# Optimization experiments

Measured on AMD Instinct MI355X. Metric: run time of the kernel, lower is better.

The kernel has to match this reference:

```python
import jax, jax.numpy as jnp
import numpy as np

FEAT_STRIDE = 16
SCALES = np.array([2.0, 4.0, 8.0, 16.0])
RATIOS = np.array([0.5, 1.0, 2.0])
TIME_DIM = (16, 12, 8, 4)
S = 16            # sample_duration
A = 12            # anchors per location = len(scales)*len(ratios)
PRE = 2000        # RPN_PRE_NMS_TOP_N (TEST)
POST = 300        # RPN_POST_NMS_TOP_N (TEST)
THRESH = 0.7      # RPN_NMS_THRESH


def _whctrs(a):
    w = a[2] - a[0] + 1.0
    h = a[3] - a[1] + 1.0
    return w, h, a[0] + 0.5 * (w - 1), a[1] + 0.5 * (h - 1)


def _mkanchors(ws, hs, xc, yc):
    ws = ws[:, None]; hs = hs[:, None]
    return np.hstack((xc - 0.5 * (ws - 1), yc - 0.5 * (hs - 1),
                      xc + 0.5 * (ws - 1), yc + 0.5 * (hs - 1)))


def generate_anchors(base_size=16):
    base = np.array([1.0, 1.0, base_size, base_size]) - 1
    w, h, xc, yc = _whctrs(base)
    ws = np.round(np.sqrt(w * h / RATIOS)); hs = np.round(ws * RATIOS)
    ratio_anchors = _mkanchors(ws, hs, xc, yc)
    rows = []
    for i in range(ratio_anchors.shape[0]):
        wi, hi, xi, yi = _whctrs(ratio_anchors[i])
        rows.append(_mkanchors(wi * SCALES, hi * SCALES, xi, yi))
    return np.vstack(rows).astype(np.float32)  # [A,4]


def _anchor_tubes(H, W):
    # spatial anchors [K*A,4] then temporal windows -> [Nw*K*A, S, 4] (static)
    base = generate_anchors()
    sx = np.arange(W) * FEAT_STRIDE; sy = np.arange(H) * FEAT_STRIDE
    X, Y = np.meshgrid(sx, sy)
    shifts = np.stack([X.ravel(), Y.ravel(), X.ravel(), Y.ravel()], 1).astype(np.float32)
    anchors = (shifts[:, None, :] + base[None]).reshape(-1, 4)  # [K*A,4]
    KA = anchors.shape[0]
    tubes = []
    for td in TIME_DIM:
        for j in range(S - td + 1):
            anc = np.zeros((S, KA, 4), np.float32)
            anc[j:j + td] = anchors
            tubes.append(anc.transpose(1, 0, 2))  # [KA,S,4]
    return np.concatenate(tubes, 0)  # [Nw*KA, S, 4]


def _gather_deltas(bboxes, B, KA):
    outs = []
    for bb, td in zip(bboxes, TIME_DIM):
        for j in range(S - td + 1):
            t = jnp.transpose(bb[:, :, j], (0, 2, 3, 1)).reshape(B, KA, td, 4)
            outs.append(jnp.pad(t, ((0, 0), (0, 0), (j, S - j - td), (0, 0))))
    return jnp.concatenate(outs, 1)  # [B, Nw*KA, S, 4]


def _bbox_transform_inv(boxes, deltas):
    w = boxes[..., 2] - boxes[..., 0] + 1.0
    h = boxes[..., 3] - boxes[..., 1] + 1.0
    cx = boxes[..., 0] + 0.5 * w
    cy = boxes[..., 1] + 0.5 * h
    pcx = deltas[..., 0] * w + cx
    pcy = deltas[..., 1] * h + cy
    pw = jnp.exp(deltas[..., 2]) * w
    ph = jnp.exp(deltas[..., 3]) * h
    return jnp.stack([pcx - 0.5 * pw, pcy - 0.5 * ph,
                      pcx + 0.5 * pw, pcy + 0.5 * ph], -1)


def _clip_boxes(b, im_info):
    imh = im_info[:, 0][:, None, None] - 1.0
    imw = im_info[:, 1][:, None, None] - 1.0
    return jnp.stack([jnp.clip(b[..., 0], 0.0, imw), jnp.clip(b[..., 1], 0.0, imh),
                      jnp.clip(b[..., 2], 0.0, imw), jnp.clip(b[..., 3], 0.0, imh)], -1)


def _nms_single(args):
    props, sc, order, bidx = args
    top = order[:PRE]
    p = props[top]                 # [PRE, S, 4]
    s = sc[top]
    pg = jax.lax.stop_gradient(p)  # NMS selection is non-differentiable
    area = jnp.sum((pg[..., 2] - pg[..., 0] + 1.0) * (pg[..., 3] - pg[..., 1] + 1.0), -1)

    def frame(inter, fb):          # fb: [PRE,4] boxes of one frame
        xx1 = jnp.maximum(fb[:, 0, None], fb[None, :, 0])
        yy1 = jnp.maximum(fb[:, 1, None], fb[None, :, 1])
        xx2 = jnp.minimum(fb[:, 2, None], fb[None, :, 2])
        yy2 = jnp.minimum(fb[:, 3, None], fb[None, :, 3])
        return inter + jnp.maximum(xx2 - xx1 + 1.0, 0.0) * jnp.maximum(yy2 - yy1 + 1.0, 0.0), None

    inter, _ = jax.lax.scan(frame, jnp.zeros((PRE, PRE), pg.dtype), jnp.transpose(pg, (1, 0, 2)))
    iou = inter / (area[:, None] + area[None, :] - inter)  # spatio-temporal tube IoU
    idxv = jnp.arange(PRE)

    def body(keep, i):
        sup = (iou[i] > THRESH) & (idxv > i)
        return jnp.where(keep[i], keep & ~sup, keep), None

    keep, _ = jax.lax.scan(body, jnp.ones(PRE, bool), idxv)
    kept = jnp.argsort(jnp.where(keep, idxv, PRE))[:POST]
    valid = (jnp.arange(POST) < jnp.minimum(keep.sum(), POST)).astype(p.dtype)
    pk = p[kept].reshape(POST, S * 4) * valid[:, None]
    sk = s[kept] * valid
    col0 = jnp.full((POST, 1), bidx, p.dtype)
    return jnp.concatenate([col0, pk, sk[:, None]], 1)  # [POST, S*4+2]


def reference(scores16, scores12, scores8, scores4, bbox16, bbox12, bbox8, bbox4, im_info):
    B, H, W = scores16.shape[0], scores16.shape[3], scores16.shape[4]
    KA = H * W * A
    slist = [t[:, A:] for t in (scores16, scores12, scores8, scores4)]
    scores_all = jnp.concatenate([jnp.transpose(t, (0, 2, 3, 4, 1)).reshape(B, -1) for t in slist], 1)
    anchors = jnp.asarray(_anchor_tubes(H, W))                       # [N,S,4]
    deltas = _gather_deltas([bbox16, bbox12, bbox8, bbox4], B, KA)   # [B,N,S,4]
    props = _clip_boxes(_bbox_transform_inv(anchors[None], deltas), im_info)
    order = jnp.argsort(-scores_all, axis=1)                         # descending
    bidx = jnp.arange(B, dtype=props.dtype)
    return jax.lax.map(_nms_single, (props, scores_all, order, bidx))  # [B,POST,S*4+2]


def setup_inputs() -> dict:
    key = jax.random.key(0)
    k = jax.random.split(key, 8)
    B, H, W = 16, 7, 7
    T = [1, 5, 9, 13]  # temporal windows per time_dim (16,12,8,4)
    scores16 = jax.random.uniform(k[0], (B, 2 * A, T[0], H, W), jnp.float32)
    scores12 = jax.random.uniform(k[1], (B, 2 * A, T[1], H, W), jnp.float32)
    scores8 = jax.random.uniform(k[2], (B, 2 * A, T[2], H, W), jnp.float32)
    scores4 = jax.random.uniform(k[3], (B, 2 * A, T[3], H, W), jnp.float32)
    bbox16 = 0.1 * jax.random.normal(k[4], (B, A * 16 * 4, T[0], H, W), jnp.float32)
    bbox12 = 0.1 * jax.random.normal(k[5], (B, A * 12 * 4, T[1], H, W), jnp.float32)
    bbox8 = 0.1 * jax.random.normal(k[6], (B, A * 8 * 4, T[2], H, W), jnp.float32)
    bbox4 = 0.1 * jax.random.normal(k[7], (B, A * 4 * 4, T[3], H, W), jnp.float32)
    im_info = jnp.ones((B, 3), jnp.float32) * jnp.array([112.0, 112.0, 1.0], jnp.float32)
    return {"scores16": scores16, "scores12": scores12, "scores8": scores8, "scores4": scores4,
            "bbox16": bbox16, "bbox12": bbox12, "bbox8": bbox8, "bbox4": bbox4, "im_info": im_info}
```

## Files before the change

kernel.cpp:

```cpp
#include <hip/hip_runtime.h>
#include <cstdint>
#include <cstddef>

#define BB   16
#define HH   7
#define WW   7
#define AA   12
#define KAA  588
#define NN   16464
#define NPAD 32768
#define PRE  2000
#define POST 300
#define SS   16

__device__ __constant__ float BASE_ANC[12][4] = {
  {-15.f,  -4.f,  30.f,  19.f},
  {-38.f, -16.f,  53.f,  31.f},
  {-84.f, -40.f,  99.f,  55.f},
  {-176.f,-88.f, 191.f, 103.f},
  {-8.f,   -8.f,  23.f,  23.f},
  {-24.f, -24.f,  39.f,  39.f},
  {-56.f, -56.f,  71.f,  71.f},
  {-120.f,-120.f,135.f, 135.f},
  {-3.f,  -14.f,  18.f,  29.f},
  {-14.f, -36.f,  29.f,  51.f},
  {-36.f, -80.f,  51.f,  95.f},
  {-80.f, -168.f, 95.f, 183.f},
};

__device__ __forceinline__ void decode_idx(int idx, int& s, int& j, int& h, int& w, int& a) {
  int local;
  if (idx < 588)       { s = 0; local = idx; }
  else if (idx < 3528) { s = 1; local = idx - 588; }
  else if (idx < 8820) { s = 2; local = idx - 3528; }
  else                 { s = 3; local = idx - 8820; }
  j = local / KAA;
  int anc = local - j * KAA;
  h = anc / (WW * AA);
  int rem = anc - h * (WW * AA);
  w = rem / AA;
  a = rem - w * AA;
}

__global__ void init_keys(const float* __restrict__ s16, const float* __restrict__ s12,
                          const float* __restrict__ s8,  const float* __restrict__ s4,
                          uint64_t* __restrict__ keys, float* __restrict__ scores) {
  int t = blockIdx.x * blockDim.x + threadIdx.x;
  int b = t >> 15;
  int slot = t & (NPAD - 1);
  uint64_t key = ~0ull;
  if (slot < NN) {
    int s, j, h, w, a;
    decode_idx(slot, s, j, h, w, a);
    const float* sp; int T;
    if (s == 0)      { sp = s16; T = 1; }
    else if (s == 1) { sp = s12; T = 5; }
    else if (s == 2) { sp = s8;  T = 9; }
    else             { sp = s4;  T = 13; }
    float sc = sp[(((b * (2*AA) + AA + a) * T + j) * HH + h) * WW + w];
    scores[b * NN + slot] = sc;
    uint32_t u = __float_as_uint(sc);
    uint32_t mono = (u & 0x80000000u) ? ~u : (u | 0x80000000u);
    key = ((uint64_t)(~mono) << 32) | (uint32_t)slot;
  }
  keys[((size_t)b << 15) + slot] = key;
}

__global__ __launch_bounds__(1024) void chunk_sort(uint64_t* __restrict__ keys) {
  __shared__ uint64_t sh[2048];
  int chunk = blockIdx.x;
  uint64_t* seg = keys + (size_t)chunk * 2048;
  int base = (chunk & 15) * 2048;
  int t = threadIdx.x;
  sh[t] = seg[t];
  sh[t + 1024] = seg[t + 1024];
  __syncthreads();
  for (int k = 2; k <= 2048; k <<= 1) {
    for (int j = k >> 1; j >= 1; j >>= 1) {
      int i = ((t & ~(j - 1)) << 1) | (t & (j - 1));
      int p = i | j;
      bool asc = (((base + i) & k) == 0);
      uint64_t x = sh[i], y = sh[p];
      bool sw = asc ? (x > y) : (x < y);
      if (sw) { sh[i] = y; sh[p] = x; }
      __syncthreads();
    }
  }
  seg[t] = sh[t];
  seg[t + 1024] = sh[t + 1024];
}

__global__ void bitonic_global(uint64_t* __restrict__ keys, int k, int j) {
  int t = blockIdx.x * blockDim.x + threadIdx.x;
  int b = t >> 14;
  int u = t & 16383;
  int i = ((u & ~(j - 1)) << 1) | (u & (j - 1));
  int p = i | j;
  bool asc = ((i & k) == 0);
  uint64_t* seg = keys + ((size_t)b << 15);
  uint64_t x = seg[i], y = seg[p];
  bool sw = asc ? (x > y) : (x < y);
  if (sw) { seg[i] = y; seg[p] = x; }
}

__global__ __launch_bounds__(1024) void bitonic_merge(uint64_t* __restrict__ keys, int k) {
  __shared__ uint64_t sh[2048];
  int chunk = blockIdx.x;
  uint64_t* seg = keys + (size_t)chunk * 2048;
  int base = (chunk & 15) * 2048;
  int t = threadIdx.x;
  sh[t] = seg[t];
  sh[t + 1024] = seg[t + 1024];
  __syncthreads();
  bool asc = ((base & k) == 0);
  for (int j = 1024; j >= 1; j >>= 1) {
    int i = ((t & ~(j - 1)) << 1) | (t & (j - 1));
    int p = i | j;
    uint64_t x = sh[i], y = sh[p];
    bool sw = asc ? (x > y) : (x < y);
    if (sw) { sh[i] = y; sh[p] = x; }
    __syncthreads();
  }
  seg[t] = sh[t];
  seg[t + 1024] = sh[t + 1024];
}

__global__ void props_kernel(const uint64_t* __restrict__ keys, const float* __restrict__ scores,
                             const float* __restrict__ bb16, const float* __restrict__ bb12,
                             const float* __restrict__ bb8,  const float* __restrict__ bb4,
                             const float* __restrict__ im_info,
                             float* __restrict__ props, float* __restrict__ area,
                             float* __restrict__ tsc) {
  int t = blockIdx.x * blockDim.x + threadIdx.x;
  if (t >= BB * PRE) return;
  int b = t / PRE;
  int r = t - b * PRE;
  int idx = (int)(keys[((size_t)b << 15) + r] & 0xffffffffu);
  int s, j, h, w, a;
  decode_idx(idx, s, j, h, w, a);
  const float* bp; int T, td, C;
  if (s == 0)      { bp = bb16; T = 1;  td = 16; C = AA*16*4; }
  else if (s == 1) { bp = bb12; T = 5;  td = 12; C = AA*12*4; }
  else if (s == 2) { bp = bb8;  T = 9;  td = 8;  C = AA*8*4;  }
  else             { bp = bb4;  T = 13; td = 4;  C = AA*4*4;  }

  float imh = im_info[b * 3 + 0] - 1.0f;
  float imw = im_info[b * 3 + 1] - 1.0f;

  float ax1 = BASE_ANC[a][0] + (float)(w * 16);
  float ay1 = BASE_ANC[a][1] + (float)(h * 16);
  float ax2 = BASE_ANC[a][2] + (float)(w * 16);
  float ay2 = BASE_ANC[a][3] + (float)(h * 16);
  float wa = ax2 - ax1 + 1.0f;
  float ha = ay2 - ay1 + 1.0f;
  float cx = ax1 + 0.5f * wa;
  float cy = ay1 + 0.5f * ha;

  int chanStride = T * HH * WW;
  float* pr = props + ((size_t)b * PRE + r) * (SS * 4);
  float acc = 0.0f;
  for (int f = 0; f < SS; ++f) {
    float x1, y1, x2, y2;
    if (f >= j && f < j + td) {
      int tt = f - j;
      int cb = (a * td + tt) * 4;
      size_t base = ((((size_t)b * C + cb) * T + j) * HH + h) * WW + w;
      float d0 = bp[base];
      float d1 = bp[base + chanStride];
      float d2 = bp[base + 2 * chanStride];
      float d3 = bp[base + 3 * chanStride];
      float pcx = d0 * wa + cx;
      float pcy = d1 * ha + cy;
      float pw = expf(d2) * wa;
      float ph = expf(d3) * ha;
      x1 = pcx - 0.5f * pw;
      y1 = pcy - 0.5f * ph;
      x2 = pcx + 0.5f * pw;
      y2 = pcy + 0.5f * ph;
    } else {
      x1 = 0.0f; y1 = 0.0f; x2 = 1.0f; y2 = 1.0f;
    }
    x1 = fminf(fmaxf(x1, 0.0f), imw);
    x2 = fminf(fmaxf(x2, 0.0f), imw);
    y1 = fminf(fmaxf(y1, 0.0f), imh);
    y2 = fminf(fmaxf(y2, 0.0f), imh);
    pr[f * 4 + 0] = x1;
    pr[f * 4 + 1] = y1;
    pr[f * 4 + 2] = x2;
    pr[f * 4 + 3] = y2;
    acc += (x2 - x1 + 1.0f) * (y2 - y1 + 1.0f);
  }
  area[b * PRE + r] = acc;
  tsc[b * PRE + r] = scores[b * NN + idx];
}

#define MITILE 128
#define MJC    8
#define MNIT   16

#define FRAME(f, Bf) { float4 r = shp[ii][f];                       \
    float xx1 = fmaxf(r.x, Bf.x); float yy1 = fmaxf(r.y, Bf.y);     \
    float xx2 = fminf(r.z, Bf.z); float yy2 = fminf(r.w, Bf.w);     \
    inter += fmaxf(xx2 - xx1 + 1.0f, 0.0f) *                        \
             fmaxf(yy2 - yy1 + 1.0f, 0.0f); }

#define KEEP4(v) asm volatile("" : "+v"(v.x), "+v"(v.y), "+v"(v.z), "+v"(v.w))

__global__ __launch_bounds__(256, 2) void mask_kernel(const float* __restrict__ props,
                                                      const float* __restrict__ area,
                                                      uint64_t* __restrict__ mask) {
  __shared__ float4 shp[MITILE][16];
  __shared__ float sha[MITILE];
  int b  = blockIdx.z;
  int it = blockIdx.y;
  int jc = blockIdx.x;
  int i0 = it * MITILE;
  if (jc * 256 + 255 <= i0) return;

  int tid = threadIdx.x;
  int wave = tid >> 6;
  int lane = tid & 63;

  const float4* srcb = (const float4*)(props + (size_t)b * PRE * 64);
  for (int u = tid; u < MITILE * 16; u += 256) {
    int row = u >> 4, q = u & 15;
    int ri = i0 + row; if (ri >= PRE) ri = PRE - 1;
    shp[row][q] = srcb[(size_t)ri * 16 + q];
  }
  if (tid < MITILE) {
    int ri = i0 + tid; if (ri >= PRE) ri = PRE - 1;
    sha[tid] = area[b * PRE + ri];
  }
  __syncthreads();

  int jw = jc * 4 + wave;
  int j  = jw * 64 + lane;
  bool jv = j < PRE;
  int rj = jv ? j : PRE - 1;
  const float4* pj = (const float4*)(props + ((size_t)b * PRE + rj) * 64);
  float4 B0  = pj[0],  B1  = pj[1],  B2  = pj[2],  B3  = pj[3];
  float4 B4  = pj[4],  B5  = pj[5],  B6  = pj[6],  B7  = pj[7];
  float4 B8  = pj[8],  B9  = pj[9],  B10 = pj[10], B11 = pj[11];
  float4 B12 = pj[12], B13 = pj[13], B14 = pj[14], B15 = pj[15];
  float aj = area[b * PRE + rj];
  KEEP4(B0);  KEEP4(B1);  KEEP4(B2);  KEEP4(B3);
  KEEP4(B4);  KEEP4(B5);  KEEP4(B6);  KEEP4(B7);
  KEEP4(B8);  KEEP4(B9);  KEEP4(B10); KEEP4(B11);
  KEEP4(B12); KEEP4(B13); KEEP4(B14); KEEP4(B15);
  asm volatile("" : "+v"(aj));

  int imax = PRE - i0; if (imax > MITILE) imax = MITILE;
  #pragma unroll 2
  for (int ii = 0; ii < imax; ++ii) {
    int i = i0 + ii;
    float ai = sha[ii];
    float inter = 0.0f;
    FRAME(0,B0)   FRAME(1,B1)   FRAME(2,B2)   FRAME(3,B3)
    FRAME(4,B4)   FRAME(5,B5)   FRAME(6,B6)   FRAME(7,B7)
    FRAME(8,B8)   FRAME(9,B9)   FRAME(10,B10) FRAME(11,B11)
    FRAME(12,B12) FRAME(13,B13) FRAME(14,B14) FRAME(15,B15)
    float iou = inter / (ai + aj - inter);
    bool bit = jv && (j > i) && (iou > 0.7f);
    unsigned long long word = __ballot(bit);
    if (lane == 0) mask[((size_t)b * PRE + i) * 32 + jw] = word;
  }
}

#define GD 20
__global__ __launch_bounds__(64) void greedy_kernel(const uint64_t* __restrict__ mask,
                                                    int* __restrict__ kept,
                                                    int* __restrict__ nkeep) {
  int b = blockIdx.x;
  int lane = threadIdx.x;
  unsigned long long keep = 0ull;
  if (lane < 31) keep = ~0ull;
  else if (lane == 31) keep = 0xFFFFull;

  const uint64_t* m = mask + (size_t)b * PRE * 32;
  const bool ld = lane < 32;

  unsigned long long buf[GD];
  #pragma unroll
  for (int d = 0; d < GD; ++d)
    buf[d] = ld ? m[(size_t)d * 32 + lane] : 0ull;

  for (int i0 = 0; i0 < PRE; i0 += GD) {
    #pragma unroll
    for (int d = 0; d < GD; ++d) {
      int i = i0 + d;
      unsigned long long cur = buf[d];
      int ip = i + GD;
      buf[d] = (ld && ip < PRE) ? m[(size_t)ip * 32 + lane] : 0ull;
      int iw = i >> 6;
      if (lane < iw) cur = 0ull;
      else if (lane == iw) cur &= ~((2ull << (i & 63)) - 1ull);
      unsigned long long kw = __shfl(keep, iw);
      if ((kw >> (i & 63)) & 1ull) {
        keep &= ~cur;
      }
    }
  }

  int pc = __popcll(keep);
  int incl = pc;
  for (int o = 1; o < 32; o <<= 1) {
    int v = __shfl_up(incl, o);
    if (lane >= o) incl += v;
  }
  int excl = incl - pc;
  int total = __shfl(incl, 31);
  if (lane < 32) {
    int rank = excl;
    unsigned long long bits = keep;
    while (bits) {
      int bpos = __ffsll(bits) - 1;
      bits &= bits - 1ull;
      if (rank < POST) kept[b * POST + rank] = lane * 64 + bpos;
      rank++;
    }
  }
  if (lane == 0) nkeep[b] = total < POST ? total : POST;
}

__global__ void out_kernel(const float* __restrict__ props, const float* __restrict__ tsc,
                           const int* __restrict__ kept, const int* __restrict__ nkeep,
                           float* __restrict__ out) {
  int t = blockIdx.x * blockDim.x + threadIdx.x;
  if (t >= BB * POST) return;
  int b = t / POST;
  int r = t - b * POST;
  float* row = out + (size_t)t * 66;
  row[0] = (float)b;
  if (r < nkeep[b]) {
    int i = kept[b * POST + r];
    const float* p = props + ((size_t)b * PRE + i) * 64;
    #pragma unroll
    for (int c = 0; c < 64; ++c) row[1 + c] = p[c];
    row[65] = tsc[b * PRE + i];
  } else {
    #pragma unroll
    for (int c = 1; c < 66; ++c) row[c] = 0.0f;
  }
}

extern "C" void kernel_launch(void* const* d_in, const int* in_sizes, int n_in,
                              void* d_out, int out_size, void* d_ws, size_t ws_size,
                              hipStream_t stream) {
  const float* s16 = (const float*)d_in[0];
  const float* s12 = (const float*)d_in[1];
  const float* s8  = (const float*)d_in[2];
  const float* s4  = (const float*)d_in[3];
  const float* b16 = (const float*)d_in[4];
  const float* b12 = (const float*)d_in[5];
  const float* b8  = (const float*)d_in[6];
  const float* b4  = (const float*)d_in[7];
  const float* imi = (const float*)d_in[8];
  float* out = (float*)d_out;

  uint8_t* w = (uint8_t*)d_ws;
  uint64_t* keys = (uint64_t*)w;  w += (size_t)BB * NPAD * 8;
  float* scores  = (float*)w;     w += (size_t)BB * NN * 4;
  float* props   = (float*)w;     w += (size_t)BB * PRE * 64 * 4;
  float* area    = (float*)w;     w += (size_t)BB * PRE * 4;
  float* tsc     = (float*)w;     w += (size_t)BB * PRE * 4;
  uint64_t* mask = (uint64_t*)w;  w += (size_t)BB * PRE * 32 * 8;
  int* kept      = (int*)w;       w += (size_t)BB * POST * 4;
  int* nkeep     = (int*)w;       w += 64;

  init_keys<<<(BB * NPAD) / 256, 256, 0, stream>>>(s16, s12, s8, s4, keys, scores);

  chunk_sort<<<BB * (NPAD / 2048), 1024, 0, stream>>>(keys);
  for (int k = 4096; k <= NPAD; k <<= 1) {
    for (int j = k >> 1; j >= 2048; j >>= 1) {
      bitonic_global<<<(BB * (NPAD / 2)) / 256, 256, 0, stream>>>(keys, k, j);
    }
    bitonic_merge<<<BB * (NPAD / 2048), 1024, 0, stream>>>(keys, k);
  }

  props_kernel<<<(BB * PRE + 255) / 256, 256, 0, stream>>>(keys, scores, b16, b12, b8, b4,
                                                           imi, props, area, tsc);
  {
    dim3 g(MJC, MNIT, BB);
    mask_kernel<<<g, 256, 0, stream>>>(props, area, mask);
  }
  greedy_kernel<<<BB, 64, 0, stream>>>(mask, kept, nkeep);
  out_kernel<<<(BB * POST + 255) / 256, 256, 0, stream>>>(props, tsc, kept, nkeep, out);
}
```

Baseline: 761.4 us.

## Restructure NMS mask kernel to per-wave tiles reading row boxes directly

Replaces the block-level shared-memory staging of i-row proposals with independent per-wave work items. Each wave handles one 64-column j word over a 125-row i chunk and loads the row boxes straight from global memory (uniform addresses, cached), which removes the __syncthreads and the LDS traffic. Grid is flattened to 2048 blocks, occupancy hint is raised to 3, and fully-below-diagonal waves exit early. The cost is repeated global/L2 reads of row data per wave, plus more register pressure from holding 16 row float4s alongside 16 column float4s.

```diff
diff --git a/kernel.cpp b/kernel.cpp
--- a/kernel.cpp
+++ b/kernel.cpp
@@ -194,46 +194,30 @@
   tsc[b * PRE + r] = scores[b * NN + idx];
 }
 
-#define MITILE 128
-#define MJC    8
-#define MNIT   16
-
-#define FRAME(f, Bf) { float4 r = shp[ii][f];                       \
-    float xx1 = fmaxf(r.x, Bf.x); float yy1 = fmaxf(r.y, Bf.y);     \
-    float xx2 = fminf(r.z, Bf.z); float yy2 = fminf(r.w, Bf.w);     \
-    inter += fmaxf(xx2 - xx1 + 1.0f, 0.0f) *                        \
-             fmaxf(yy2 - yy1 + 1.0f, 0.0f); }
-
+#define MICHUNK 125
 #define KEEP4(v) asm volatile("" : "+v"(v.x), "+v"(v.y), "+v"(v.z), "+v"(v.w))
 
-__global__ __launch_bounds__(256, 2) void mask_kernel(const float* __restrict__ props,
+#define SFRAME(Rq, Bf) { \
+    float xx1 = fmaxf(Rq.x, Bf.x); \
+    float yy1 = fmaxf(Rq.y, Bf.y); \
+    float xx2 = fminf(Rq.z, Bf.z); \
+    float yy2 = fminf(Rq.w, Bf.w); \
+    inter += fmaxf(xx2 - xx1 + 1.0f, 0.0f) * fmaxf(yy2 - yy1 + 1.0f, 0.0f); }
+
+__global__ __launch_bounds__(256, 3) void mask_kernel(const float* __restrict__ props,
                                                       const float* __restrict__ area,
                                                       uint64_t* __restrict__ mask) {
-  __shared__ float4 shp[MITILE][16];
-  __shared__ float sha[MITILE];
-  int b  = blockIdx.z;
-  int it = blockIdx.y;
-  int jc = blockIdx.x;
-  int i0 = it * MITILE;
-  if (jc * 256 + 255 <= i0) return;
-
-  int tid = threadIdx.x;
-  int wave = tid >> 6;
-  int lane = tid & 63;
-
-  const float4* srcb = (const float4*)(props + (size_t)b * PRE * 64);
-  for (int u = tid; u < MITILE * 16; u += 256) {
-    int row = u >> 4, q = u & 15;
-    int ri = i0 + row; if (ri >= PRE) ri = PRE - 1;
-    shp[row][q] = srcb[(size_t)ri * 16 + q];
-  }
-  if (tid < MITILE) {
-    int ri = i0 + tid; if (ri >= PRE) ri = PRE - 1;
-    sha[tid] = area[b * PRE + ri];
-  }
-  __syncthreads();
-
-  int jw = jc * 4 + wave;
+  int bid  = blockIdx.x;
+  int b    = bid >> 7;
+  int rem  = bid & 127;
+  int wave = threadIdx.x >> 6;
+  int lane = threadIdx.x & 63;
+  int wid  = rem * 4 + wave;
+  int jw   = wid & 31;
+  int ic   = wid >> 5;
+  int is   = ic * MICHUNK;
+  if (jw * 64 + 63 <= is) return;
+
   int j  = jw * 64 + lane;
   bool jv = j < PRE;
   int rj = jv ? j : PRE - 1;
@@ -249,20 +233,29 @@
   KEEP4(B12); KEEP4(B13); KEEP4(B14); KEEP4(B15);
   asm volatile("" : "+v"(aj));
 
-  int imax = PRE - i0; if (imax > MITILE) imax = MITILE;
-  #pragma unroll 2
-  for (int ii = 0; ii < imax; ++ii) {
-    int i = i0 + ii;
-    float ai = sha[ii];
+  const float4* rows  = (const float4*)(props + (size_t)b * PRE * 64);
+  const float* area_b = area + b * PRE;
+  uint64_t* mcol = mask + (size_t)b * PRE * 32 + jw;
+
+  int ie = is + MICHUNK;
+  #pragma unroll 1
+  for (int i = is; i < ie; ++i) {
+    const float4* rp = rows + (size_t)i * 16;
+    float4 R0  = rp[0],  R1  = rp[1],  R2  = rp[2],  R3  = rp[3];
+    float4 R4  = rp[4],  R5  = rp[5],  R6  = rp[6],  R7  = rp[7];
+    float4 R8  = rp[8],  R9  = rp[9],  R10 = rp[10], R11 = rp[11];
+    float4 R12 = rp[12], R13 = rp[13], R14 = rp[14], R15 = rp[15];
+    float ai = area_b[i];
+
     float inter = 0.0f;
-    FRAME(0,B0)   FRAME(1,B1)   FRAME(2,B2)   FRAME(3,B3)
-    FRAME(4,B4)   FRAME(5,B5)   FRAME(6,B6)   FRAME(7,B7)
-    FRAME(8,B8)   FRAME(9,B9)   FRAME(10,B10) FRAME(11,B11)
-    FRAME(12,B12) FRAME(13,B13) FRAME(14,B14) FRAME(15,B15)
+    SFRAME(R0,B0)   SFRAME(R1,B1)   SFRAME(R2,B2)   SFRAME(R3,B3)
+    SFRAME(R4,B4)   SFRAME(R5,B5)   SFRAME(R6,B6)   SFRAME(R7,B7)
+    SFRAME(R8,B8)   SFRAME(R9,B9)   SFRAME(R10,B10) SFRAME(R11,B11)
+    SFRAME(R12,B12) SFRAME(R13,B13) SFRAME(R14,B14) SFRAME(R15,B15)
     float iou = inter / (ai + aj - inter);
     bool bit = jv && (j > i) && (iou > 0.7f);
     unsigned long long word = __ballot(bit);
-    if (lane == 0) mask[((size_t)b * PRE + i) * 32 + jw] = word;
+    if (lane == 0) mcol[(size_t)i * 32] = word;
   }
 }
 
@@ -379,10 +372,7 @@
 
   props_kernel<<<(BB * PRE + 255) / 256, 256, 0, stream>>>(keys, scores, b16, b12, b8, b4,
                                                            imi, props, area, tsc);
-  {
-    dim3 g(MJC, MNIT, BB);
-    mask_kernel<<<g, 256, 0, stream>>>(props, area, mask);
-  }
+  mask_kernel<<<2048, 256, 0, stream>>>(props, area, mask);
   greedy_kernel<<<BB, 64, 0, stream>>>(mask, kept, nkeep);
   out_kernel<<<(BB * POST + 255) / 256, 256, 0, stream>>>(props, tsc, kept, nkeep, out);
 }
```

After: 1.081 ms. 41.9% more time.

## Replace full bitonic sort with top-2048 pairwise merge reduction

Applied to the files above, without the earlier changes.

Each 2048-key chunk is now sorted ascending. The global bitonic stages are replaced by four merge_top launches. Each launch combines two sorted runs: it loads the second run reversed into shared memory, keeps the element-wise minimum of the two halves, and bitonic-cleans the result so only the smallest 2048 keys stay in place. Since only the first PRE=2000 keys are used later, this skips sorting the full 32768-key segment per batch and cuts many small kernel launches. The trade-off is that later merge levels run on very few blocks (down to one block per batch), which leaves the device mostly idle during those steps.

```diff
diff --git a/kernel.cpp b/kernel.cpp
--- a/kernel.cpp
+++ b/kernel.cpp
@@ -70,7 +70,6 @@
   __shared__ uint64_t sh[2048];
   int chunk = blockIdx.x;
   uint64_t* seg = keys + (size_t)chunk * 2048;
-  int base = (chunk & 15) * 2048;
   int t = threadIdx.x;
   sh[t] = seg[t];
   sh[t + 1024] = seg[t + 1024];
@@ -79,7 +78,7 @@
     for (int j = k >> 1; j >= 1; j >>= 1) {
       int i = ((t & ~(j - 1)) << 1) | (t & (j - 1));
       int p = i | j;
-      bool asc = (((base + i) & k) == 0);
+      bool asc = ((i & k) == 0);
       uint64_t x = sh[i], y = sh[p];
       bool sw = asc ? (x > y) : (x < y);
       if (sw) { sh[i] = y; sh[p] = x; }
@@ -90,39 +89,36 @@
   seg[t + 1024] = sh[t + 1024];
 }
 
-__global__ void bitonic_global(uint64_t* __restrict__ keys, int k, int j) {
-  int t = blockIdx.x * blockDim.x + threadIdx.x;
-  int b = t >> 14;
-  int u = t & 16383;
-  int i = ((u & ~(j - 1)) << 1) | (u & (j - 1));
-  int p = i | j;
-  bool asc = ((i & k) == 0);
-  uint64_t* seg = keys + ((size_t)b << 15);
-  uint64_t x = seg[i], y = seg[p];
-  bool sw = asc ? (x > y) : (x < y);
-  if (sw) { seg[i] = y; seg[p] = x; }
-}
-
-__global__ __launch_bounds__(1024) void bitonic_merge(uint64_t* __restrict__ keys, int k) {
-  __shared__ uint64_t sh[2048];
-  int chunk = blockIdx.x;
-  uint64_t* seg = keys + (size_t)chunk * 2048;
-  int base = (chunk & 15) * 2048;
+__global__ __launch_bounds__(1024) void merge_top(uint64_t* __restrict__ keys,
+                                                  int nmerge, int span) {
+  __shared__ uint64_t sh[4096];
+  int bid = blockIdx.x;
+  int b = bid / nmerge;
+  int m = bid - b * nmerge;
+  uint64_t* A = keys + ((size_t)b << 15) + (size_t)m * (2 * span);
+  const uint64_t* Bp = A + span;
   int t = threadIdx.x;
-  sh[t] = seg[t];
-  sh[t + 1024] = seg[t + 1024];
+  sh[t] = A[t];
+  sh[t + 1024] = A[t + 1024];
+  sh[4095 - t] = Bp[t];
+  sh[3071 - t] = Bp[t + 1024];
   __syncthreads();
-  bool asc = ((base & k) == 0);
+  {
+    uint64_t x0 = sh[t], y0 = sh[t + 2048];
+    if (y0 < x0) sh[t] = y0;
+    uint64_t x1 = sh[t + 1024], y1 = sh[t + 3072];
+    if (y1 < x1) sh[t + 1024] = y1;
+  }
+  __syncthreads();
   for (int j = 1024; j >= 1; j >>= 1) {
     int i = ((t & ~(j - 1)) << 1) | (t & (j - 1));
     int p = i | j;
     uint64_t x = sh[i], y = sh[p];
-    bool sw = asc ? (x > y) : (x < y);
-    if (sw) { sh[i] = y; sh[p] = x; }
+    if (x > y) { sh[i] = y; sh[p] = x; }
     __syncthreads();
   }
-  seg[t] = sh[t];
-  seg[t + 1024] = sh[t + 1024];
+  A[t] = sh[t];
+  A[t + 1024] = sh[t + 1024];
 }
 
 __global__ void props_kernel(const uint64_t* __restrict__ keys, const float* __restrict__ scores,
@@ -370,12 +366,10 @@
   init_keys<<<(BB * NPAD) / 256, 256, 0, stream>>>(s16, s12, s8, s4, keys, scores);
 
   chunk_sort<<<BB * (NPAD / 2048), 1024, 0, stream>>>(keys);
-  for (int k = 4096; k <= NPAD; k <<= 1) {
-    for (int j = k >> 1; j >= 2048; j >>= 1) {
-      bitonic_global<<<(BB * (NPAD / 2)) / 256, 256, 0, stream>>>(keys, k, j);
-    }
-    bitonic_merge<<<BB * (NPAD / 2048), 1024, 0, stream>>>(keys, k);
-  }
+  merge_top<<<BB * 8, 1024, 0, stream>>>(keys, 8, 2048);
+  merge_top<<<BB * 4, 1024, 0, stream>>>(keys, 4, 4096);
+  merge_top<<<BB * 2, 1024, 0, stream>>>(keys, 2, 8192);
+  merge_top<<<BB * 1, 1024, 0, stream>>>(keys, 1, 16384);
 
   props_kernel<<<(BB * PRE + 255) / 256, 256, 0, stream>>>(keys, scores, b16, b12, b8, b4,
                                                            imi, props, area, tsc);
```

Measured after the change: 736.0 us. 3.3% less time.
